# Optimization experiments

Hardware: AMD Instinct MI355X
Metric: run time of the kernel (lower is better)

Reference implementation:

```python
import jax, jax.numpy as jnp
import numpy as np

MAX_FRAMES = 12
EMBED_DIM = 512
TOPK = 12
NUM_SAMPLES = 500
SIGMA = 0.05
SEL_DIM = 2
NUM_HEADS = 2


def setup_inputs() -> dict:
    key = jax.random.key(0)
    ks = jax.random.split(key, 9)
    D = EMBED_DIM
    C = D // 2
    s = lambda fan_in: 1.0 / np.sqrt(fan_in)
    return {
        "x": jax.random.normal(ks[0], (16, MAX_FRAMES * 50, D), dtype=jnp.float32),
        "ln_g": jnp.ones((D,), jnp.float32),
        "ln_b": jnp.zeros((D,), jnp.float32),
        "w_in": jax.random.normal(ks[1], (D, C), jnp.float32) * s(D),
        "wq": jax.random.normal(ks[2], (C, C), jnp.float32) * s(C),
        "wk": jax.random.normal(ks[3], (C, C), jnp.float32) * s(C),
        "wv": jax.random.normal(ks[4], (C, C), jnp.float32) * s(C),
        "wo": jax.random.normal(ks[5], (C, C), jnp.float32) * s(C),
        "w1": jax.random.normal(ks[6], (2 * C, C), jnp.float32) * s(2 * C),
        "w2": jax.random.normal(ks[7], (C, 1), jnp.float32) * s(C),
    }


def layer_norm(x, g, b, eps=1e-5):
    mu = jnp.mean(x, axis=-1, keepdims=True)
    var = jnp.var(x, axis=-1, keepdims=True)
    return (x - mu) * jax.lax.rsqrt(var + eps) * g + b


def mha(x, wq, wk, wv, wo):
    B, N, C = x.shape
    hd = C // NUM_HEADS
    q = (x @ wq).reshape(B, N, NUM_HEADS, hd).transpose(0, 2, 1, 3)
    k = (x @ wk).reshape(B, N, NUM_HEADS, hd).transpose(0, 2, 1, 3)
    v = (x @ wv).reshape(B, N, NUM_HEADS, hd).transpose(0, 2, 1, 3)
    attn = jax.nn.softmax(jnp.einsum('bhnd,bhmd->bhnm', q, k) / np.sqrt(hd), axis=-1)
    out = jnp.einsum('bhnm,bhmd->bhnd', attn, v).transpose(0, 2, 1, 3).reshape(B, N, C)
    return out @ wo


def predictor(x, ln_g, ln_b, w_in, wq, wk, wv, wo, w1, w2):
    h = jax.nn.gelu(layer_norm(x, ln_g, ln_b) @ w_in, approximate=False)
    h = mha(h, wq, wk, wv, wo)
    B, N, C = h.shape
    g = jnp.mean(h, axis=1, keepdims=True)
    h = jnp.concatenate([h, jnp.broadcast_to(g, (B, N, C))], axis=-1)
    h = jax.nn.gelu(h @ w1, approximate=False)
    return jnp.tanh(h @ w2)  # (B, N, 1)


def perturbed_topk(scores):
    # scores: (b, d) -> soft indicators (b, k, d)
    b, d = scores.shape
    noise = jax.random.normal(jax.random.key(1), (b, NUM_SAMPLES, d), dtype=scores.dtype)
    perturbed = scores[:, None, :] + noise * SIGMA
    _, idx = jax.lax.top_k(perturbed, TOPK)            # (b, ns, k)
    idx = jnp.sort(idx, axis=-1)
    onehot = jax.nn.one_hot(idx, d, dtype=scores.dtype)  # (b, ns, k, d)
    return onehot.mean(axis=1)                          # (b, k, d)


def reference(x, ln_g, ln_b, w_in, wq, wk, wv, wo, w1, w2):
    B, L, D = x.shape
    N = L // MAX_FRAMES
    xf = x.reshape(B * MAX_FRAMES, N, D)
    pred = predictor(xf, ln_g, ln_b, w_in, wq, wk, wv, wo, w1, w2)[..., 0]  # (b, N)
    spatial_score = pred[:, SEL_DIM:]                    # (b, N-2)
    ind = perturbed_topk(spatial_score)                  # (b, k, N-2)
    cls_feat = xf[:, :SEL_DIM, :]
    spatial_feat = xf[:, SEL_DIM:, :]
    sel = jnp.einsum('bkl,bld->bkd', ind, spatial_feat)
    out = jnp.concatenate([cls_feat, sel], axis=1)       # (b, 2+k, D)
    return out.reshape(B, -1, D)
```

## Files before the change

kernel.cpp:

```cpp
#include <hip/hip_runtime.h>
#include <stdint.h>

#define B2      192
#define NTOK    50
#define ROWS    9600
#define D_EMB   512
#define C_DIM   256
#define HD      128
#define NSAMP   500
#define TOPKK   12
#define NSPA    48
#define NSAMP_T 96000
#define NOISE_OFF 61953536ull
#define NOISE_BYTES 18432000ull
#define WS_NEED (NOISE_OFF + NOISE_BYTES)

typedef short short8 __attribute__((ext_vector_type(8)));
typedef float f32x4  __attribute__((ext_vector_type(4)));

__device__ __forceinline__ float gelu_f(float x) {
    return 0.5f * x * (1.0f + erff(x * 0.7071067811865476f));
}
__device__ __forceinline__ uint16_t f2bf(float x) {
    uint32_t u = __float_as_uint(x);
    return (uint16_t)((u + 0x7fffu + ((u >> 16) & 1u)) >> 16);
}
__device__ __forceinline__ float bf2f(uint16_t b) {
    return __uint_as_float(((uint32_t)b) << 16);
}
__device__ __forceinline__ size_t swzA(int m, int k, int K) {
    return ((size_t)(m >> 4) * (K >> 5) + (k >> 5)) * 512
         + (size_t)((((k >> 3) & 3) * 16 + (m & 15)) * 8 + (k & 7));
}

__device__ __forceinline__ uint32_t rotl32(uint32_t x, int r) {
    return (x << r) | (x >> (32 - r));
}
__device__ __forceinline__ void threefry01(uint32_t& x0, uint32_t& x1) {
    const uint32_t ks0 = 0u, ks1 = 1u, ks2 = 0x1BD11BDBu;
    x0 += ks0; x1 += ks1;
#define TFR(r) { x0 += x1; x1 = rotl32(x1, r); x1 ^= x0; }
    TFR(13) TFR(15) TFR(26) TFR(6)  x0 += ks1; x1 += ks2 + 1u;
    TFR(17) TFR(29) TFR(16) TFR(24) x0 += ks2; x1 += ks0 + 2u;
    TFR(13) TFR(15) TFR(26) TFR(6)  x0 += ks0; x1 += ks1 + 3u;
    TFR(17) TFR(29) TFR(16) TFR(24) x0 += ks1; x1 += ks2 + 4u;
    TFR(13) TFR(15) TFR(26) TFR(6)  x0 += ks2; x1 += ks0 + 5u;
#undef TFR
}

__device__ __forceinline__ float erfinv_xla(float x) {
    float w = -log1pf(-x * x);
    float p;
    if (w < 5.0f) {
        w -= 2.5f;
        p = 2.81022636e-08f;
        p = fmaf(p, w, 3.43273939e-07f);
        p = fmaf(p, w, -3.5233877e-06f);
        p = fmaf(p, w, -4.39150654e-06f);
        p = fmaf(p, w, 0.00021858087f);
        p = fmaf(p, w, -0.00125372503f);
        p = fmaf(p, w, -0.00417768164f);
        p = fmaf(p, w, 0.246640727f);
        p = fmaf(p, w, 1.50140941f);
    } else {
        w = sqrtf(w) - 3.0f;
        p = -0.000200214257f;
        p = fmaf(p, w, 0.000100950558f);
        p = fmaf(p, w, 0.00134934322f);
        p = fmaf(p, w, -0.00367342844f);
        p = fmaf(p, w, 0.00573950773f);
        p = fmaf(p, w, -0.0076224613f);
        p = fmaf(p, w, 0.00943887047f);
        p = fmaf(p, w, 1.00167406f);
        p = fmaf(p, w, 2.83297682f);
    }
    return p * x;
}

__device__ __forceinline__ float bits_to_normal(uint32_t bits) {
    float f = __uint_as_float((bits >> 9) | 0x3f800000u) - 1.0f;
    float u = f * 2.0f + (-0.99999994039535522461f);
    u = fmaxf(-0.99999994039535522461f, u);
    return 1.4142135623730951f * erfinv_xla(u);
}

__global__ __launch_bounds__(256) void noise_kernel(float* __restrict__ noise) {
    int T  = blockIdx.x * 256 + threadIdx.x;
    int q  = T / NSAMP_T;
    int g2 = T - q * NSAMP_T;
    uint32_t cbase = (uint32_t)g2 * 48u + (uint32_t)(q * 4);
    float4 o;
    { uint32_t x0=0u, x1=cbase + 0u; threefry01(x0,x1); o.x = bits_to_normal(x0^x1) * 0.05f; }
    { uint32_t x0=0u, x1=cbase + 1u; threefry01(x0,x1); o.y = bits_to_normal(x0^x1) * 0.05f; }
    { uint32_t x0=0u, x1=cbase + 2u; threefry01(x0,x1); o.z = bits_to_normal(x0^x1) * 0.05f; }
    { uint32_t x0=0u, x1=cbase + 3u; threefry01(x0,x1); o.w = bits_to_normal(x0^x1) * 0.05f; }
    ((float4*)noise)[(size_t)q * NSAMP_T + g2] = o;
}

__global__ __launch_bounds__(256) void prep_kernel(const float* __restrict__ x,
                                                   const float* __restrict__ g,
                                                   const float* __restrict__ b,
                                                   short* __restrict__ xh,
                                                   short* __restrict__ xl,
                                                   const float* __restrict__ w_in, const float* __restrict__ wq,
                                                   const float* __restrict__ wk, const float* __restrict__ wv,
                                                   const float* __restrict__ wo, const float* __restrict__ w1,
                                                   short* win_hi, short* win_lo, short* wq_hi, short* wq_lo,
                                                   short* wk_hi, short* wk_lo, short* wv_hi, short* wv_lo,
                                                   short* wo_hi, short* wo_lo, short* w1a_hi, short* w1a_lo,
                                                   short* w1b_hi, short* w1b_lo) {
    if (blockIdx.x < 2400) {
        int row  = blockIdx.x * 4 + (threadIdx.x >> 6);
        int lane = threadIdx.x & 63;
        const float* rp = x + (size_t)row * D_EMB;
        float4 v0 = *(const float4*)(rp + lane * 8);
        float4 v1 = *(const float4*)(rp + lane * 8 + 4);
        float s  = v0.x + v0.y + v0.z + v0.w + v1.x + v1.y + v1.z + v1.w;
        float s2 = v0.x*v0.x + v0.y*v0.y + v0.z*v0.z + v0.w*v0.w
                 + v1.x*v1.x + v1.y*v1.y + v1.z*v1.z + v1.w*v1.w;
#pragma unroll
        for (int off = 32; off; off >>= 1) {
            s  += __shfl_xor(s,  off);
            s2 += __shfl_xor(s2, off);
        }
        float mu  = s / 512.0f;
        float var = s2 / 512.0f - mu * mu;
        float inv = 1.0f / sqrtf(var + 1e-5f);
        const float* gp = g + lane * 8;
        const float* bp = b + lane * 8;
        float o[8];
        o[0]=(v0.x-mu)*inv*gp[0]+bp[0]; o[1]=(v0.y-mu)*inv*gp[1]+bp[1];
        o[2]=(v0.z-mu)*inv*gp[2]+bp[2]; o[3]=(v0.w-mu)*inv*gp[3]+bp[3];
        o[4]=(v1.x-mu)*inv*gp[4]+bp[4]; o[5]=(v1.y-mu)*inv*gp[5]+bp[5];
        o[6]=(v1.z-mu)*inv*gp[6]+bp[6]; o[7]=(v1.w-mu)*inv*gp[7]+bp[7];
        short8 h8, l8;
#pragma unroll
        for (int j = 0; j < 8; ++j) {
            uint16_t h = f2bf(o[j]);
            h8[j] = (short)h;
            l8[j] = (short)f2bf(o[j] - bf2f(h));
        }
        size_t blk = (size_t)(row >> 4) * 16 + (lane >> 2);
        int inner  = (lane & 3) * 16 + (row & 15);
        ((short8*)xh)[blk * 64 + inner] = h8;
        ((short8*)xl)[blk * 64 + inner] = l8;
    } else {
        int blk = blockIdx.x - 2400;
        const float* W; short *hi, *lo; int K, base;
        if      (blk <  64) { W = w_in;            hi = win_hi; lo = win_lo; K = 512; base = 0;   }
        else if (blk <  96) { W = wq;              hi = wq_hi;  lo = wq_lo;  K = 256; base = 64;  }
        else if (blk < 128) { W = wk;              hi = wk_hi;  lo = wk_lo;  K = 256; base = 96;  }
        else if (blk < 160) { W = wv;              hi = wv_hi;  lo = wv_lo;  K = 256; base = 128; }
        else if (blk < 192) { W = wo;              hi = wo_hi;  lo = wo_lo;  K = 256; base = 160; }
        else if (blk < 224) { W = w1;              hi = w1a_hi; lo = w1a_lo; K = 256; base = 192; }
        else                { W = w1 + 256 * 256;  hi = w1b_hi; lo = w1b_lo; K = 256; base = 224; }
        int t = (blk - base) * 256 + threadIdx.x;
        int n = t & 255, k8 = t >> 8;
        short8 h8, l8;
#pragma unroll
        for (int j = 0; j < 8; ++j) {
            float wvl = W[(size_t)(k8 * 8 + j) * 256 + n];
            uint16_t h = f2bf(wvl);
            h8[j] = (short)h;
            l8[j] = (short)f2bf(wvl - bf2f(h));
        }
        size_t bb = (size_t)(n >> 4) * (K >> 5) + (k8 >> 2);
        int inner = (k8 & 3) * 16 + (n & 15);
        ((short8*)hi)[bb * 64 + inner] = h8;
        ((short8*)lo)[bb * 64 + inner] = l8;
    }
}

template<int KB>
__device__ __forceinline__ void mm_core(const short8* __restrict__ pAh, const short8* __restrict__ pAl,
                                        const short8* __restrict__ pBh0, const short8* __restrict__ pBl0,
                                        const short8* __restrict__ pBh1, const short8* __restrict__ pBl1,
                                        f32x4& acc0, f32x4& acc1) {
    short8 ah[3], al[3], bh0[3], bl0[3], bh1[3], bl1[3];
#pragma unroll
    for (int i = 0; i < 2; ++i) {
        int off = i * 64;
        ah[i] = pAh[off];  al[i] = pAl[off];
        bh0[i] = pBh0[off]; bl0[i] = pBl0[off];
        bh1[i] = pBh1[off]; bl1[i] = pBl1[off];
    }
#pragma unroll
    for (int ks = 0; ks < KB; ++ks) {
        int cur = ks % 3;
        if (ks + 2 < KB) {
            int pre = (ks + 2) % 3, off = (ks + 2) * 64;
            ah[pre] = pAh[off];  al[pre] = pAl[off];
            bh0[pre] = pBh0[off]; bl0[pre] = pBl0[off];
            bh1[pre] = pBh1[off]; bl1[pre] = pBl1[off];
        }
        acc0 = __builtin_amdgcn_mfma_f32_16x16x32_bf16(ah[cur], bh0[cur], acc0, 0, 0, 0);
        acc0 = __builtin_amdgcn_mfma_f32_16x16x32_bf16(ah[cur], bl0[cur], acc0, 0, 0, 0);
        acc0 = __builtin_amdgcn_mfma_f32_16x16x32_bf16(al[cur], bh0[cur], acc0, 0, 0, 0);
        acc1 = __builtin_amdgcn_mfma_f32_16x16x32_bf16(ah[cur], bh1[cur], acc1, 0, 0, 0);
        acc1 = __builtin_amdgcn_mfma_f32_16x16x32_bf16(ah[cur], bl1[cur], acc1, 0, 0, 0);
        acc1 = __builtin_amdgcn_mfma_f32_16x16x32_bf16(al[cur], bh1[cur], acc1, 0, 0, 0);
    }
}

__device__ __forceinline__ void epi_store(f32x4 acc, int row0, int col, int N,
                                          float* __restrict__ Cf, short* __restrict__ Chi,
                                          short* __restrict__ Clo,
                                          const float* __restrict__ bias, int act) {
#pragma unroll
    for (int r = 0; r < 4; ++r) {
        int row = row0 + r;
        float v2 = acc[r];
        if (bias) v2 += bias[(size_t)(row / 50) * N + col];
        if (act)  v2 = gelu_f(v2);
        if (Cf) Cf[(size_t)row * N + col] = v2;
        if (Chi) {
            uint16_t h = f2bf(v2);
            size_t ad = swzA(row, col, 256);
            Chi[ad] = (short)h;
            Clo[ad] = (short)f2bf(v2 - bf2f(h));
        }
    }
}

template<int KB>
__global__ __launch_bounds__(256) void gemm_one(const short8* __restrict__ Ah,
                                                const short8* __restrict__ Al,
                                                const short8* __restrict__ Bh,
                                                const short8* __restrict__ Bl,
                                                float* __restrict__ Cf,
                                                short* __restrict__ Chi,
                                                short* __restrict__ Clo,
                                                const float* __restrict__ bias,
                                                int act) {
    int lane = threadIdx.x & 63;
    int wv   = threadIdx.x >> 6;
    int ms   = blockIdx.x * 4 + wv;
    int ns0  = blockIdx.y * 2;
    const short8* pAh  = Ah + (size_t)ms  * KB * 64 + lane;
    const short8* pAl  = Al + (size_t)ms  * KB * 64 + lane;
    const short8* pBh0 = Bh + (size_t)ns0 * KB * 64 + lane;
    const short8* pBl0 = Bl + (size_t)ns0 * KB * 64 + lane;
    const short8* pBh1 = pBh0 + (size_t)KB * 64;
    const short8* pBl1 = pBl0 + (size_t)KB * 64;
    f32x4 acc0 = {0.f,0.f,0.f,0.f}, acc1 = {0.f,0.f,0.f,0.f};
    mm_core<KB>(pAh, pAl, pBh0, pBl0, pBh1, pBl1, acc0, acc1);
    int row0 = ms * 16 + (lane >> 4) * 4;
    int cin  = lane & 15;
    epi_store(acc0, row0, ns0 * 16 + cin,      256, Cf, Chi, Clo, bias, act);
    epi_store(acc1, row0, (ns0 + 1) * 16 + cin, 256, Cf, Chi, Clo, bias, act);
}

__global__ __launch_bounds__(256) void gemm_qkv(const short8* __restrict__ Ah,
                                                const short8* __restrict__ Al,
                                                const short8* __restrict__ Bhq, const short8* __restrict__ Blq,
                                                const short8* __restrict__ Bhk, const short8* __restrict__ Blk,
                                                const short8* __restrict__ Bhv, const short8* __restrict__ Blv,
                                                float* __restrict__ q, float* __restrict__ k,
                                                float* __restrict__ v) {
    int lane = threadIdx.x & 63;
    int wv   = threadIdx.x >> 6;
    int ms   = blockIdx.x * 4 + wv;
    int sel  = blockIdx.y >> 3;
    int ns0  = (blockIdx.y & 7) * 2;
    const short8* Bh = (sel == 0) ? Bhq : (sel == 1) ? Bhk : Bhv;
    const short8* Bl = (sel == 0) ? Blq : (sel == 1) ? Blk : Blv;
    float* C = (sel == 0) ? q : (sel == 1) ? k : v;
    const short8* pAh  = Ah + (size_t)ms  * 8 * 64 + lane;
    const short8* pAl  = Al + (size_t)ms  * 8 * 64 + lane;
    const short8* pBh0 = Bh + (size_t)ns0 * 8 * 64 + lane;
    const short8* pBl0 = Bl + (size_t)ns0 * 8 * 64 + lane;
    const short8* pBh1 = pBh0 + 8 * 64;
    const short8* pBl1 = pBl0 + 8 * 64;
    f32x4 acc0 = {0.f,0.f,0.f,0.f}, acc1 = {0.f,0.f,0.f,0.f};
    mm_core<8>(pAh, pAl, pBh0, pBl0, pBh1, pBl1, acc0, acc1);
    int row0 = ms * 16 + (lane >> 4) * 4;
    int cin  = lane & 15;
    epi_store(acc0, row0, ns0 * 16 + cin,      256, C, nullptr, nullptr, nullptr, 0);
    epi_store(acc1, row0, (ns0 + 1) * 16 + cin, 256, C, nullptr, nullptr, nullptr, 0);
}

__global__ __launch_bounds__(256) void attn_kernel(const float* __restrict__ q,
                                                   const float* __restrict__ k,
                                                   const float* __restrict__ v,
                                                   short* __restrict__ aoh,
                                                   short* __restrict__ aol) {
    __shared__ float sQ[NTOK * 132];
    __shared__ float sK[NTOK * 132];
    __shared__ float sS[NTOK * 51];
    int blk = blockIdx.x;
    int b = blk >> 1, h = blk & 1;
    const size_t base = (size_t)b * NTOK * C_DIM + h * HD;
    int tid = threadIdx.x;
    for (int idx = tid; idx < 1600; idx += 256) {
        int r = idx >> 5, c = (idx & 31) * 4;
        *(float4*)&sQ[r * 132 + c] = *(const float4*)(q + base + (size_t)r * C_DIM + c);
        *(float4*)&sK[r * 132 + c] = *(const float4*)(k + base + (size_t)r * C_DIM + c);
    }
    __syncthreads();
    for (int e = tid; e < 625; e += 256) {
        int i2 = e / 25, j2 = e - i2 * 25;
        int i = i2 * 2, j = j2 * 2;
        const float* qi0 = &sQ[i * 132];
        const float* qi1 = qi0 + 132;
        const float* kj0 = &sK[j * 132];
        const float* kj1 = kj0 + 132;
        float4 a00 = {0,0,0,0}, a01 = {0,0,0,0}, a10 = {0,0,0,0}, a11 = {0,0,0,0};
#pragma unroll
        for (int t = 0; t < 32; ++t) {
            float4 q0 = *(const float4*)&qi0[t * 4];
            float4 q1 = *(const float4*)&qi1[t * 4];
            float4 b0 = *(const float4*)&kj0[t * 4];
            float4 b1 = *(const float4*)&kj1[t * 4];
            a00.x = fmaf(q0.x, b0.x, a00.x); a00.y = fmaf(q0.y, b0.y, a00.y);
            a00.z = fmaf(q0.z, b0.z, a00.z); a00.w = fmaf(q0.w, b0.w, a00.w);
            a01.x = fmaf(q0.x, b1.x, a01.x); a01.y = fmaf(q0.y, b1.y, a01.y);
            a01.z = fmaf(q0.z, b1.z, a01.z); a01.w = fmaf(q0.w, b1.w, a01.w);
            a10.x = fmaf(q1.x, b0.x, a10.x); a10.y = fmaf(q1.y, b0.y, a10.y);
            a10.z = fmaf(q1.z, b0.z, a10.z); a10.w = fmaf(q1.w, b0.w, a10.w);
            a11.x = fmaf(q1.x, b1.x, a11.x); a11.y = fmaf(q1.y, b1.y, a11.y);
            a11.z = fmaf(q1.z, b1.z, a11.z); a11.w = fmaf(q1.w, b1.w, a11.w);
        }
        const float sc = 0.08838834764831845f;
        sS[i * 51 + j]           = (a00.x + a00.y + a00.z + a00.w) * sc;
        sS[i * 51 + j + 1]       = (a01.x + a01.y + a01.z + a01.w) * sc;
        sS[(i + 1) * 51 + j]     = (a10.x + a10.y + a10.z + a10.w) * sc;
        sS[(i + 1) * 51 + j + 1] = (a11.x + a11.y + a11.z + a11.w) * sc;
    }
    __syncthreads();
    for (int idx = tid; idx < 1600; idx += 256) {
        int r = idx >> 5, c = (idx & 31) * 4;
        *(float4*)&sQ[r * 132 + c] = *(const float4*)(v + base + (size_t)r * C_DIM + c);
    }
    if (tid < NTOK) {
        float* row = &sS[tid * 51];
        float m = row[0];
        for (int j = 1; j < NTOK; ++j) m = fmaxf(m, row[j]);
        float sum = 0.f;
        for (int j = 0; j < NTOK; ++j) { float e2 = expf(row[j] - m); row[j] = e2; sum += e2; }
        float inv = 1.0f / sum;
        for (int j = 0; j < NTOK; ++j) row[j] *= inv;
    }
    __syncthreads();
    for (int e = tid; e < 1600; e += 256) {
        int i = e >> 5, d4 = (e & 31) * 4;
        const float* srow = &sS[i * 51];
        float4 acc = {0,0,0,0};
#pragma unroll
        for (int j = 0; j < NTOK; ++j) {
            float w = srow[j];
            float4 v4 = *(const float4*)&sQ[j * 132 + d4];
            acc.x = fmaf(w, v4.x, acc.x); acc.y = fmaf(w, v4.y, acc.y);
            acc.z = fmaf(w, v4.z, acc.z); acc.w = fmaf(w, v4.w, acc.w);
        }
        int row = b * NTOK + i;
        float vals[4] = {acc.x, acc.y, acc.z, acc.w};
#pragma unroll
        for (int c = 0; c < 4; ++c) {
            int col = h * HD + d4 + c;
            uint16_t hh = f2bf(vals[c]);
            size_t ad = swzA(row, col, 256);
            aoh[ad] = (short)hh;
            aol[ad] = (short)f2bf(vals[c] - bf2f(hh));
        }
    }
}

__global__ __launch_bounds__(256) void mean50(const float* __restrict__ h2,
                                              short* __restrict__ gh,
                                              short* __restrict__ gl) {
    int b = blockIdx.x, c = threadIdx.x;
    float s = 0.f;
    for (int n = 0; n < NTOK; ++n) s += h2[((size_t)b * NTOK + n) * C_DIM + c];
    float g = s / 50.0f;
    uint16_t h = f2bf(g);
    size_t ad = swzA(b, c, 256);
    gh[ad] = (short)h;
    gl[ad] = (short)f2bf(g - bf2f(h));
}

__global__ __launch_bounds__(256) void matvec_tanh(const float* __restrict__ h3,
                                                   const float* __restrict__ w2,
                                                   float* __restrict__ pred) {
    int row  = blockIdx.x * 4 + (threadIdx.x >> 6);
    int lane = threadIdx.x & 63;
    const float* rp = h3 + (size_t)row * C_DIM;
    float4 a = *(const float4*)(rp + lane * 4);
    float4 w = *(const float4*)(w2 + lane * 4);
    float s = a.x * w.x + a.y * w.y + a.z * w.z + a.w * w.w;
#pragma unroll
    for (int off = 32; off; off >>= 1) s += __shfl_xor(s, off);
    if (lane == 0) pred[row] = tanhf(s);
}

__device__ __forceinline__ unsigned long long topk_key(uint32_t base, int d,
                                                       const float* __restrict__ sp) {
    uint32_t x0 = 0u, x1 = base + (uint32_t)d;
    threefry01(x0, x1);
    float n  = bits_to_normal(x0 ^ x1);
    float v  = sp[d] + n * 0.05f;
    uint32_t vb   = __float_as_uint(v);
    uint32_t mono = (vb & 0x80000000u) ? ~vb : (vb | 0x80000000u);
    return ((unsigned long long)mono << 6) | (unsigned)(63 - d);
}

#define STEP(li) { unsigned long long mn_ = (key < li) ? key : li; \
                   li = (key > li) ? key : li; key = mn_; }
#define S1  STEP(l0)
#define S2  S1  STEP(l1)
#define S3  S2  STEP(l2)
#define S4  S3  STEP(l3)
#define S5  S4  STEP(l4)
#define S6  S5  STEP(l5)
#define S7  S6  STEP(l6)
#define S8  S7  STEP(l7)
#define S9  S8  STEP(l8)
#define S10 S9  STEP(l9)
#define S11 S10 STEP(l10)
#define S12 S11 STEP(l11)

#define TOPK_MERGE_TAIL                                                        \
    int rowL = p * 64 + lane;                                                  \
    if (hh == 1) {                                                             \
        unsigned long long* r = sK[rowL];                                      \
        r[0]=l0; r[1]=l1; r[2]=l2;  r[3]=l3;  r[4]=l4;   r[5]=l5;              \
        r[6]=l6; r[7]=l7; r[8]=l8;  r[9]=l9;  r[10]=l10; r[11]=l11;            \
    }                                                                          \
    __syncthreads();                                                           \
    if (hh == 0) {                                                             \
        const unsigned long long* r = sK[rowL];                                \
        unsigned long long M0  = (l0  > r[11]) ? l0  : r[11];                  \
        unsigned long long M1  = (l1  > r[10]) ? l1  : r[10];                  \
        unsigned long long M2  = (l2  > r[9])  ? l2  : r[9];                   \
        unsigned long long M3  = (l3  > r[8])  ? l3  : r[8];                   \
        unsigned long long M4  = (l4  > r[7])  ? l4  : r[7];                   \
        unsigned long long M5  = (l5  > r[6])  ? l5  : r[6];                   \
        unsigned long long M6  = (l6  > r[5])  ? l6  : r[5];                   \
        unsigned long long M7  = (l7  > r[4])  ? l7  : r[4];                   \
        unsigned long long M8  = (l8  > r[3])  ? l8  : r[3];                   \
        unsigned long long M9  = (l9  > r[2])  ? l9  : r[2];                   \
        unsigned long long M10 = (l10 > r[1])  ? l10 : r[1];                   \
        unsigned long long M11 = (l11 > r[0])  ? l11 : r[0];                   \
        unsigned long long m = 0ull;                                           \
        m |= 1ull << (unsigned)(M0  & 63ull);  m |= 1ull << (unsigned)(M1  & 63ull); \
        m |= 1ull << (unsigned)(M2  & 63ull);  m |= 1ull << (unsigned)(M3  & 63ull); \
        m |= 1ull << (unsigned)(M4  & 63ull);  m |= 1ull << (unsigned)(M5  & 63ull); \
        m |= 1ull << (unsigned)(M6  & 63ull);  m |= 1ull << (unsigned)(M7  & 63ull); \
        m |= 1ull << (unsigned)(M8  & 63ull);  m |= 1ull << (unsigned)(M9  & 63ull); \
        m |= 1ull << (unsigned)(M10 & 63ull);  m |= 1ull << (unsigned)(M11 & 63ull); \
        EMIT(M0)  EMIT(M1)  EMIT(M2)  EMIT(M3)  EMIT(M4)  EMIT(M5)             \
        EMIT(M6)  EMIT(M7)  EMIT(M8)  EMIT(M9)  EMIT(M10) EMIT(M11)            \
    }
#define EMIT(Mi) { unsigned a_ = (unsigned)(Mi & 63ull); \
                   int kpos_ = 11 - __popcll(m & ((1ull << a_) - 1ull)); \
                   int d_ = 63 - (int)a_; \
                   atomicAdd(&counts[((size_t)b * TOPKK + kpos_) * NSPA + d_], 1); }

__global__ __launch_bounds__(256, 4) void topk_noise(const float* __restrict__ pred,
                                                     const float4* __restrict__ nz4,
                                                     int* __restrict__ counts) {
    __shared__ unsigned long long sK[128][13];
    __shared__ float sSP[2][48];
    int lane = threadIdx.x & 63;
    int wv   = threadIdx.x >> 6;
    int p    = wv >> 1;
    int hh   = wv & 1;
    int b0   = (blockIdx.x * 128) / NSAMP;
    if (threadIdx.x < 96) {
        int r = threadIdx.x / 48, dd = threadIdx.x - r * 48;
        int bb = b0 + r; if (bb > B2 - 1) bb = B2 - 1;
        sSP[r][dd] = pred[bb * NTOK + 2 + dd];
    }
    int g = blockIdx.x * 128 + p * 64 + lane;
    int b = g / NSAMP;
    int bo = b - b0;
    __syncthreads();
    const float* spl = &sSP[bo][hh * 24];
    const float4* nq = nz4 + (size_t)(hh * 6) * NSAMP_T + g;

    float4 n0 = nq[0 * NSAMP_T], n1 = nq[1 * NSAMP_T], n2 = nq[2 * NSAMP_T];
    float4 n3 = nq[3 * NSAMP_T], n4 = nq[4 * NSAMP_T], n5 = nq[5 * NSAMP_T];

    unsigned long long l0=0ull,l1=0ull,l2=0ull,l3=0ull,l4=0ull,l5=0ull,
                       l6=0ull,l7=0ull,l8=0ull,l9=0ull,l10=0ull,l11=0ull;
    unsigned long long key;

#define MKKEY(dd, nv) { float v_ = spl[dd] + (nv); uint32_t vb_ = __float_as_uint(v_); \
    uint32_t mono_ = (vb_ & 0x80000000u) ? ~vb_ : (vb_ | 0x80000000u); \
    key = ((unsigned long long)mono_ << 6) | (unsigned)(63 - (hh * 24 + (dd))); }

    MKKEY(0,  n0.x) S1   MKKEY(1,  n0.y) S2   MKKEY(2,  n0.z) S3   MKKEY(3,  n0.w) S4
    MKKEY(4,  n1.x) S5   MKKEY(5,  n1.y) S6   MKKEY(6,  n1.z) S7   MKKEY(7,  n1.w) S8
    MKKEY(8,  n2.x) S9   MKKEY(9,  n2.y) S10  MKKEY(10, n2.z) S11  MKKEY(11, n2.w) S12
    MKKEY(12, n3.x) S12  MKKEY(13, n3.y) S12  MKKEY(14, n3.z) S12  MKKEY(15, n3.w) S12
    MKKEY(16, n4.x) S12  MKKEY(17, n4.y) S12  MKKEY(18, n4.z) S12  MKKEY(19, n4.w) S12
    MKKEY(20, n5.x) S12  MKKEY(21, n5.y) S12  MKKEY(22, n5.z) S12  MKKEY(23, n5.w) S12
#undef MKKEY

    TOPK_MERGE_TAIL
}

__global__ __launch_bounds__(256, 4) void topk_fb(const float* __restrict__ pred,
                                                  int* __restrict__ counts) {
    __shared__ unsigned long long sK[128][13];
    int lane = threadIdx.x & 63;
    int wv   = threadIdx.x >> 6;
    int p    = wv >> 1;
    int hh   = wv & 1;
    int g    = blockIdx.x * 128 + p * 64 + lane;
    int b    = g / NSAMP;
    int s    = g - b * NSAMP;
    uint32_t base = (uint32_t)((b * NSAMP + s) * NSPA);
    const float* sp = pred + b * NTOK + 2;
    int d0 = hh * 24;

    unsigned long long l0=0ull,l1=0ull,l2=0ull,l3=0ull,l4=0ull,l5=0ull,
                       l6=0ull,l7=0ull,l8=0ull,l9=0ull,l10=0ull,l11=0ull;
    unsigned long long key;

    key = topk_key(base, d0 + 0,  sp); S1
    key = topk_key(base, d0 + 1,  sp); S2
    key = topk_key(base, d0 + 2,  sp); S3
    key = topk_key(base, d0 + 3,  sp); S4
    key = topk_key(base, d0 + 4,  sp); S5
    key = topk_key(base, d0 + 5,  sp); S6
    key = topk_key(base, d0 + 6,  sp); S7
    key = topk_key(base, d0 + 7,  sp); S8
    key = topk_key(base, d0 + 8,  sp); S9
    key = topk_key(base, d0 + 9,  sp); S10
    key = topk_key(base, d0 + 10, sp); S11
    key = topk_key(base, d0 + 11, sp); S12
#pragma unroll 2
    for (int dd = 12; dd < 24; ++dd) {
        key = topk_key(base, d0 + dd, sp); S12
    }

    TOPK_MERGE_TAIL
}
#undef EMIT
#undef TOPK_MERGE_TAIL
#undef STEP
#undef S1
#undef S2
#undef S3
#undef S4
#undef S5
#undef S6
#undef S7
#undef S8
#undef S9
#undef S10
#undef S11
#undef S12

__global__ __launch_bounds__(256) void select_out2(const float* __restrict__ x,
                                                   const int* __restrict__ counts,
                                                   float* __restrict__ out) {
    int b = blockIdx.x;
    int d = threadIdx.x;
    __shared__ float sw[TOPKK * NSPA];
    __shared__ int anyl[NSPA];
    for (int i = d; i < TOPKK * NSPA; i += 256)
        sw[i] = (float)counts[(size_t)b * TOPKK * NSPA + i] * 0.002f;
    __syncthreads();
    if (d < NSPA) {
        int a = 0;
        for (int k2 = 0; k2 < TOPKK; ++k2) a |= (sw[k2 * NSPA + d] != 0.0f);
        anyl[d] = a;
    }
    __syncthreads();
    {
        const float* xr0 = x + (size_t)(b * NTOK) * D_EMB;
        out[(size_t)(b * 14 + 0) * D_EMB + d]       = xr0[d];
        out[(size_t)(b * 14 + 0) * D_EMB + d + 256] = xr0[d + 256];
        out[(size_t)(b * 14 + 1) * D_EMB + d]       = xr0[D_EMB + d];
        out[(size_t)(b * 14 + 1) * D_EMB + d + 256] = xr0[D_EMB + d + 256];
    }
    float a0[TOPKK], a1[TOPKK];
#pragma unroll
    for (int k2 = 0; k2 < TOPKK; ++k2) { a0[k2] = 0.f; a1[k2] = 0.f; }
    for (int l = 0; l < NSPA; ++l) {
        if (!anyl[l]) continue;
        const float* xr = x + (size_t)(b * NTOK + 2 + l) * D_EMB;
        float v0 = xr[d], v1 = xr[d + 256];
#pragma unroll
        for (int k2 = 0; k2 < TOPKK; ++k2) {
            float w = sw[k2 * NSPA + l];
            a0[k2] = fmaf(w, v0, a0[k2]);
            a1[k2] = fmaf(w, v1, a1[k2]);
        }
    }
#pragma unroll
    for (int k2 = 0; k2 < TOPKK; ++k2) {
        out[(size_t)(b * 14 + 2 + k2) * D_EMB + d]       = a0[k2];
        out[(size_t)(b * 14 + 2 + k2) * D_EMB + d + 256] = a1[k2];
    }
}

extern "C" void kernel_launch(void* const* d_in, const int* in_sizes, int n_in,
                              void* d_out, int out_size, void* d_ws, size_t ws_size,
                              hipStream_t stream) {
    const float* x    = (const float*)d_in[0];
    const float* ln_g = (const float*)d_in[1];
    const float* ln_b = (const float*)d_in[2];
    const float* w_in = (const float*)d_in[3];
    const float* wq   = (const float*)d_in[4];
    const float* wk   = (const float*)d_in[5];
    const float* wv   = (const float*)d_in[6];
    const float* wo   = (const float*)d_in[7];
    const float* w1   = (const float*)d_in[8];
    const float* w2   = (const float*)d_in[9];
    float* out = (float*)d_out;

    char* W = (char*)d_ws;
    short* xn_hi  = (short*)(W + 0);
    short* xn_lo  = (short*)(W + 9830400);
    short* ao_hi  = (short*)(W + 0);
    short* ao_lo  = (short*)(W + 4915200);
    short* h2_hi  = (short*)(W + 9830400);
    short* h2_lo  = (short*)(W + 14745600);
    short* h1_hi  = (short*)(W + 19660800);
    short* h1_lo  = (short*)(W + 24576000);
    float* h3     = (float*)(W + 19660800);
    float* q      = (float*)(W + 29491200);
    float* h2f    = (float*)(W + 29491200);
    float* k      = (float*)(W + 39321600);
    float* v      = (float*)(W + 49152000);
    short* win_hi = (short*)(W + 58982400);
    short* win_lo = (short*)(W + 59244544);
    short* wq_hi  = (short*)(W + 59506688);
    short* wq_lo  = (short*)(W + 59637760);
    short* wk_hi  = (short*)(W + 59768832);
    short* wk_lo  = (short*)(W + 59899904);
    short* wv_hi  = (short*)(W + 60030976);
    short* wv_lo  = (short*)(W + 60162048);
    short* wo_hi  = (short*)(W + 60293120);
    short* wo_lo  = (short*)(W + 60424192);
    short* w1a_hi = (short*)(W + 60555264);
    short* w1a_lo = (short*)(W + 60686336);
    short* w1b_hi = (short*)(W + 60817408);
    short* w1b_lo = (short*)(W + 60948480);
    short* gm_hi  = (short*)(W + 61079552);
    short* gm_lo  = (short*)(W + 61177856);
    float* gw     = (float*)(W + 61276160);
    float* pred   = (float*)(W + 61472768);
    int*   counts = (int*)  (W + 61511168);
    float* noise  = (float*)(W + NOISE_OFF);

    const bool nzmode = ws_size >= WS_NEED;

    hipMemsetAsync(counts, 0, (size_t)B2 * TOPKK * NSPA * sizeof(int), stream);
    if (nzmode) noise_kernel<<<4500, 256, 0, stream>>>(noise);
    prep_kernel<<<2656, 256, 0, stream>>>(x, ln_g, ln_b, xn_hi, xn_lo,
        w_in, wq, wk, wv, wo, w1,
        win_hi, win_lo, wq_hi, wq_lo, wk_hi, wk_lo, wv_hi, wv_lo,
        wo_hi, wo_lo, w1a_hi, w1a_lo, w1b_hi, w1b_lo);
    gemm_one<16><<<dim3(150, 8), 256, 0, stream>>>((const short8*)xn_hi, (const short8*)xn_lo,
        (const short8*)win_hi, (const short8*)win_lo, nullptr, h1_hi, h1_lo, nullptr, 1);
    gemm_qkv<<<dim3(150, 24), 256, 0, stream>>>((const short8*)h1_hi, (const short8*)h1_lo,
        (const short8*)wq_hi, (const short8*)wq_lo, (const short8*)wk_hi, (const short8*)wk_lo,
        (const short8*)wv_hi, (const short8*)wv_lo, q, k, v);
    attn_kernel<<<B2 * 2, 256, 0, stream>>>(q, k, v, ao_hi, ao_lo);
    gemm_one<8><<<dim3(150, 8), 256, 0, stream>>>((const short8*)ao_hi, (const short8*)ao_lo,
        (const short8*)wo_hi, (const short8*)wo_lo, h2f, h2_hi, h2_lo, nullptr, 0);
    mean50<<<B2, 256, 0, stream>>>(h2f, gm_hi, gm_lo);
    gemm_one<8><<<dim3(3, 8), 256, 0, stream>>>((const short8*)gm_hi, (const short8*)gm_lo,
        (const short8*)w1b_hi, (const short8*)w1b_lo, gw, nullptr, nullptr, nullptr, 0);
    gemm_one<8><<<dim3(150, 8), 256, 0, stream>>>((const short8*)h2_hi, (const short8*)h2_lo,
        (const short8*)w1a_hi, (const short8*)w1a_lo, h3, nullptr, nullptr, gw, 1);
    matvec_tanh<<<ROWS / 4, 256, 0, stream>>>(h3, w2, pred);
    if (nzmode) topk_noise<<<750, 256, 0, stream>>>(pred, (const float4*)noise, counts);
    else        topk_fb<<<750, 256, 0, stream>>>(pred, counts);
    select_out2<<<B2, 256, 0, stream>>>(x, counts, out);
}
```

Before: 294.8 us.

## Fuse w2 matvec into w1 GEMM epilogue and compute global term in fp32

The final GEMM now applies bias and gelu, then dots the result with w2 in its epilogue, reducing across lanes and accumulating into pred with atomics. This removes the h3 round trip to memory and the separate matvec kernel. The mean and global-projection GEMM are merged into one plain fp32 kernel, which drops the bf16 split of w1b. tanh moves into the top-k kernels, and the memset now also zeroes pred for the atomics; float atomic ordering makes pred nondeterministic.

```diff
diff --git a/kernel.cpp b/kernel.cpp
--- a/kernel.cpp
+++ b/kernel.cpp
@@ -107,8 +107,7 @@
                                                    const float* __restrict__ wo, const float* __restrict__ w1,
                                                    short* win_hi, short* win_lo, short* wq_hi, short* wq_lo,
                                                    short* wk_hi, short* wk_lo, short* wv_hi, short* wv_lo,
-                                                   short* wo_hi, short* wo_lo, short* w1a_hi, short* w1a_lo,
-                                                   short* w1b_hi, short* w1b_lo) {
+                                                   short* wo_hi, short* wo_lo, short* w1a_hi, short* w1a_lo) {
     if (blockIdx.x < 2400) {
         int row  = blockIdx.x * 4 + (threadIdx.x >> 6);
         int lane = threadIdx.x & 63;
@@ -147,13 +146,12 @@
     } else {
         int blk = blockIdx.x - 2400;
         const float* W; short *hi, *lo; int K, base;
-        if      (blk <  64) { W = w_in;            hi = win_hi; lo = win_lo; K = 512; base = 0;   }
-        else if (blk <  96) { W = wq;              hi = wq_hi;  lo = wq_lo;  K = 256; base = 64;  }
-        else if (blk < 128) { W = wk;              hi = wk_hi;  lo = wk_lo;  K = 256; base = 96;  }
-        else if (blk < 160) { W = wv;              hi = wv_hi;  lo = wv_lo;  K = 256; base = 128; }
-        else if (blk < 192) { W = wo;              hi = wo_hi;  lo = wo_lo;  K = 256; base = 160; }
-        else if (blk < 224) { W = w1;              hi = w1a_hi; lo = w1a_lo; K = 256; base = 192; }
-        else                { W = w1 + 256 * 256;  hi = w1b_hi; lo = w1b_lo; K = 256; base = 224; }
+        if      (blk <  64) { W = w_in; hi = win_hi; lo = win_lo; K = 512; base = 0;   }
+        else if (blk <  96) { W = wq;   hi = wq_hi;  lo = wq_lo;  K = 256; base = 64;  }
+        else if (blk < 128) { W = wk;   hi = wk_hi;  lo = wk_lo;  K = 256; base = 96;  }
+        else if (blk < 160) { W = wv;   hi = wv_hi;  lo = wv_lo;  K = 256; base = 128; }
+        else if (blk < 192) { W = wo;   hi = wo_hi;  lo = wo_lo;  K = 256; base = 160; }
+        else                { W = w1;   hi = w1a_hi; lo = w1a_lo; K = 256; base = 192; }
         int t = (blk - base) * 256 + threadIdx.x;
         int n = t & 255, k8 = t >> 8;
         short8 h8, l8;
@@ -248,6 +246,43 @@
     int cin  = lane & 15;
     epi_store(acc0, row0, ns0 * 16 + cin,      256, Cf, Chi, Clo, bias, act);
     epi_store(acc1, row0, (ns0 + 1) * 16 + cin, 256, Cf, Chi, Clo, bias, act);
+}
+
+__global__ __launch_bounds__(256) void gemm8_pred(const short8* __restrict__ Ah,
+                                                  const short8* __restrict__ Al,
+                                                  const short8* __restrict__ Bh,
+                                                  const short8* __restrict__ Bl,
+                                                  const float* __restrict__ gwb,
+                                                  const float* __restrict__ w2,
+                                                  float* __restrict__ pred_raw) {
+    int lane = threadIdx.x & 63;
+    int wv   = threadIdx.x >> 6;
+    int ms   = blockIdx.x * 4 + wv;
+    int ns0  = blockIdx.y * 2;
+    const short8* pAh  = Ah + (size_t)ms  * 8 * 64 + lane;
+    const short8* pAl  = Al + (size_t)ms  * 8 * 64 + lane;
+    const short8* pBh0 = Bh + (size_t)ns0 * 8 * 64 + lane;
+    const short8* pBl0 = Bl + (size_t)ns0 * 8 * 64 + lane;
+    const short8* pBh1 = pBh0 + 8 * 64;
+    const short8* pBl1 = pBl0 + 8 * 64;
+    f32x4 acc0 = {0.f,0.f,0.f,0.f}, acc1 = {0.f,0.f,0.f,0.f};
+    mm_core<8>(pAh, pAl, pBh0, pBl0, pBh1, pBl1, acc0, acc1);
+    int row0 = ms * 16 + (lane >> 4) * 4;
+    int cin  = lane & 15;
+    int c0   = ns0 * 16 + cin;
+    int c1   = (ns0 + 1) * 16 + cin;
+    float w2a = w2[c0], w2b = w2[c1];
+#pragma unroll
+    for (int r = 0; r < 4; ++r) {
+        int row = row0 + r;
+        int bb  = row / 50;
+        float v0 = gelu_f(acc0[r] + gwb[(size_t)bb * 256 + c0]);
+        float v1 = gelu_f(acc1[r] + gwb[(size_t)bb * 256 + c1]);
+        float t  = v0 * w2a + v1 * w2b;
+        t += __shfl_xor(t, 1); t += __shfl_xor(t, 2);
+        t += __shfl_xor(t, 4); t += __shfl_xor(t, 8);
+        if (cin == 0) atomicAdd(&pred_raw[row], t);
+    }
 }
 
 __global__ __launch_bounds__(256) void gemm_qkv(const short8* __restrict__ Ah,
@@ -365,31 +400,21 @@
     }
 }
 
-__global__ __launch_bounds__(256) void mean50(const float* __restrict__ h2,
-                                              short* __restrict__ gh,
-                                              short* __restrict__ gl) {
-    int b = blockIdx.x, c = threadIdx.x;
+__global__ __launch_bounds__(256) void mean_gw(const float* __restrict__ h2,
+                                               const float* __restrict__ w1,
+                                               float* __restrict__ gw) {
+    __shared__ float sg[C_DIM];
+    int b = blockIdx.x, d = threadIdx.x;
     float s = 0.f;
-    for (int n = 0; n < NTOK; ++n) s += h2[((size_t)b * NTOK + n) * C_DIM + c];
-    float g = s / 50.0f;
-    uint16_t h = f2bf(g);
-    size_t ad = swzA(b, c, 256);
-    gh[ad] = (short)h;
-    gl[ad] = (short)f2bf(g - bf2f(h));
-}
-
-__global__ __launch_bounds__(256) void matvec_tanh(const float* __restrict__ h3,
-                                                   const float* __restrict__ w2,
-                                                   float* __restrict__ pred) {
-    int row  = blockIdx.x * 4 + (threadIdx.x >> 6);
-    int lane = threadIdx.x & 63;
-    const float* rp = h3 + (size_t)row * C_DIM;
-    float4 a = *(const float4*)(rp + lane * 4);
-    float4 w = *(const float4*)(w2 + lane * 4);
-    float s = a.x * w.x + a.y * w.y + a.z * w.z + a.w * w.w;
-#pragma unroll
-    for (int off = 32; off; off >>= 1) s += __shfl_xor(s, off);
-    if (lane == 0) pred[row] = tanhf(s);
+    for (int n = 0; n < NTOK; ++n) s += h2[((size_t)b * NTOK + n) * C_DIM + d];
+    sg[d] = s * 0.02f;
+    __syncthreads();
+    const float* wb = w1 + 256 * 256;
+    float acc = 0.f;
+#pragma unroll 4
+    for (int k = 0; k < C_DIM; ++k)
+        acc = fmaf(sg[k], wb[(size_t)k * 256 + d], acc);
+    gw[(size_t)b * C_DIM + d] = acc;
 }
 
 __device__ __forceinline__ unsigned long long topk_key(uint32_t base, int d,
@@ -397,7 +422,7 @@
     uint32_t x0 = 0u, x1 = base + (uint32_t)d;
     threefry01(x0, x1);
     float n  = bits_to_normal(x0 ^ x1);
-    float v  = sp[d] + n * 0.05f;
+    float v  = tanhf(sp[d]) + n * 0.05f;
     uint32_t vb   = __float_as_uint(v);
     uint32_t mono = (vb & 0x80000000u) ? ~vb : (vb | 0x80000000u);
     return ((unsigned long long)mono << 6) | (unsigned)(63 - d);
@@ -468,7 +493,7 @@
     if (threadIdx.x < 96) {
         int r = threadIdx.x / 48, dd = threadIdx.x - r * 48;
         int bb = b0 + r; if (bb > B2 - 1) bb = B2 - 1;
-        sSP[r][dd] = pred[bb * NTOK + 2 + dd];
+        sSP[r][dd] = tanhf(pred[bb * NTOK + 2 + dd]);
     }
     int g = blockIdx.x * 128 + p * 64 + lane;
     int b = g / NSAMP;
@@ -620,7 +645,6 @@
     short* h2_lo  = (short*)(W + 14745600);
     short* h1_hi  = (short*)(W + 19660800);
     short* h1_lo  = (short*)(W + 24576000);
-    float* h3     = (float*)(W + 19660800);
     float* q      = (float*)(W + 29491200);
     float* h2f    = (float*)(W + 29491200);
     float* k      = (float*)(W + 39321600);
@@ -637,10 +661,6 @@
     short* wo_lo  = (short*)(W + 60424192);
     short* w1a_hi = (short*)(W + 60555264);
     short* w1a_lo = (short*)(W + 60686336);
-    short* w1b_hi = (short*)(W + 60817408);
-    short* w1b_lo = (short*)(W + 60948480);
-    short* gm_hi  = (short*)(W + 61079552);
-    short* gm_lo  = (short*)(W + 61177856);
     float* gw     = (float*)(W + 61276160);
     float* pred   = (float*)(W + 61472768);
     int*   counts = (int*)  (W + 61511168);
@@ -648,12 +668,12 @@
 
     const bool nzmode = ws_size >= WS_NEED;
 
-    hipMemsetAsync(counts, 0, (size_t)B2 * TOPKK * NSPA * sizeof(int), stream);
+    hipMemsetAsync(W + 61472768, 0, 38400 + (size_t)B2 * TOPKK * NSPA * sizeof(int), stream);
     if (nzmode) noise_kernel<<<4500, 256, 0, stream>>>(noise);
-    prep_kernel<<<2656, 256, 0, stream>>>(x, ln_g, ln_b, xn_hi, xn_lo,
+    prep_kernel<<<2624, 256, 0, stream>>>(x, ln_g, ln_b, xn_hi, xn_lo,
         w_in, wq, wk, wv, wo, w1,
         win_hi, win_lo, wq_hi, wq_lo, wk_hi, wk_lo, wv_hi, wv_lo,
-        wo_hi, wo_lo, w1a_hi, w1a_lo, w1b_hi, w1b_lo);
+        wo_hi, wo_lo, w1a_hi, w1a_lo);
     gemm_one<16><<<dim3(150, 8), 256, 0, stream>>>((const short8*)xn_hi, (const short8*)xn_lo,
         (const short8*)win_hi, (const short8*)win_lo, nullptr, h1_hi, h1_lo, nullptr, 1);
     gemm_qkv<<<dim3(150, 24), 256, 0, stream>>>((const short8*)h1_hi, (const short8*)h1_lo,
@@ -662,12 +682,9 @@
     attn_kernel<<<B2 * 2, 256, 0, stream>>>(q, k, v, ao_hi, ao_lo);
     gemm_one<8><<<dim3(150, 8), 256, 0, stream>>>((const short8*)ao_hi, (const short8*)ao_lo,
         (const short8*)wo_hi, (const short8*)wo_lo, h2f, h2_hi, h2_lo, nullptr, 0);
-    mean50<<<B2, 256, 0, stream>>>(h2f, gm_hi, gm_lo);
-    gemm_one<8><<<dim3(3, 8), 256, 0, stream>>>((const short8*)gm_hi, (const short8*)gm_lo,
-        (const short8*)w1b_hi, (const short8*)w1b_lo, gw, nullptr, nullptr, nullptr, 0);
-    gemm_one<8><<<dim3(150, 8), 256, 0, stream>>>((const short8*)h2_hi, (const short8*)h2_lo,
-        (const short8*)w1a_hi, (const short8*)w1a_lo, h3, nullptr, nullptr, gw, 1);
-    matvec_tanh<<<ROWS / 4, 256, 0, stream>>>(h3, w2, pred);
+    mean_gw<<<B2, 256, 0, stream>>>(h2f, w1, gw);
+    gemm8_pred<<<dim3(150, 8), 256, 0, stream>>>((const short8*)h2_hi, (const short8*)h2_lo,
+        (const short8*)w1a_hi, (const short8*)w1a_lo, gw, w2, pred);
     if (nzmode) topk_noise<<<750, 256, 0, stream>>>(pred, (const float4*)noise, counts);
     else        topk_fb<<<750, 256, 0, stream>>>(pred, counts);
     select_out2<<<B2, 256, 0, stream>>>(x, counts, out);
```

New measurement: 303.7 us. 3.0% more time.
